# Kernel optimization log

Hardware: AMD Instinct MI355X
Metric: run time of the kernel (lower is better)

The kernel has to match this reference:

```python
import jax, jax.numpy as jnp
import numpy as np

N_NODES = 40000
N_EDGES = 640000
N_FEAT = 128
HIDDEN = 128
N_GRAPHS = 64


def _sage_conv(x, src, dst, Wl, b, Wr):
    # PyG SAGEConv (aggr='mean', root_weight=True, normalize=False):
    # out_i = W_l @ mean_{j in N(i)} x_j + b + W_r @ x_i
    msg = x[src]                                             # [E, F]
    s = jax.ops.segment_sum(msg, dst, num_segments=N_NODES)  # [N, F]
    deg = jax.ops.segment_sum(jnp.ones((src.shape[0],), x.dtype), dst,
                              num_segments=N_NODES)
    agg = s / jnp.maximum(deg, 1.0)[:, None]
    return agg @ Wl + b + x @ Wr


def setup_inputs() -> dict:
    key = jax.random.key(0)
    ks = jax.random.split(key, 12)
    sc = 1.0 / np.sqrt(N_FEAT)
    x = jax.random.normal(ks[0], (N_NODES, N_FEAT), dtype=jnp.float32)
    edge_index = jax.random.randint(ks[1], (2, N_EDGES), 0, N_NODES, dtype=jnp.int32)
    batch = jnp.sort(jax.random.randint(ks[2], (N_NODES,), 0, N_GRAPHS, dtype=jnp.int32))
    mk = lambda k, shp: (jax.random.normal(k, shp, dtype=jnp.float32) * sc)
    return {
        'x': x, 'edge_index': edge_index, 'batch': batch,
        'W1l': mk(ks[3], (N_FEAT, HIDDEN)), 'b1': jnp.zeros((HIDDEN,), jnp.float32),
        'W1r': mk(ks[4], (N_FEAT, HIDDEN)),
        'W2l': mk(ks[5], (HIDDEN, HIDDEN)), 'b2': jnp.zeros((HIDDEN,), jnp.float32),
        'W2r': mk(ks[6], (HIDDEN, HIDDEN)),
        'W3l': mk(ks[7], (HIDDEN, HIDDEN)), 'b3': jnp.zeros((HIDDEN,), jnp.float32),
        'W3r': mk(ks[8], (HIDDEN, HIDDEN)),
        'Wlin': mk(ks[9], (3 * HIDDEN, HIDDEN)), 'blin': jnp.zeros((HIDDEN,), jnp.float32),
    }


def reference(x, edge_index, batch, W1l, b1, W1r, W2l, b2, W2r, W3l, b3, W3r, Wlin, blin):
    src, dst = edge_index[0], edge_index[1]
    h1 = jax.nn.relu(_sage_conv(x, src, dst, W1l, b1, W1r))
    h2 = jax.nn.relu(_sage_conv(h1, src, dst, W2l, b2, W2r))
    h3 = jax.nn.relu(_sage_conv(h2, src, dst, W3l, b3, W3r))
    h = jnp.concatenate([h1, h2, h3], axis=1)                # [N, 3*H]
    pooled = jax.ops.segment_sum(h, batch, num_segments=N_GRAPHS)  # global_add_pool
    out = jax.nn.relu(pooled @ Wlin + blin)                  # [G, H]
    return out
```

## Files before the change

kernel.cpp:

```cpp
#include <hip/hip_runtime.h>
#include <hip/hip_bf16.h>

#define N_NODES 40000
#define N_EDGES 640000
#define NFEAT 128
#define NGRAPHS 64
#define ECAP 1024

typedef __attribute__((ext_vector_type(8))) short short8;
typedef __attribute__((ext_vector_type(4))) float float4v;
typedef __attribute__((ext_vector_type(2))) float float2v;

static __device__ __forceinline__ float bf2f(unsigned short u) {
    unsigned int x = ((unsigned int)u) << 16;
    return __builtin_bit_cast(float, x);
}
static __device__ __forceinline__ unsigned short f2bf(float f) {
    unsigned int x = __builtin_bit_cast(unsigned int, f);
    unsigned int r = x + 0x7fffu + ((x >> 16) & 1u);
    return (unsigned short)(r >> 16);
}

__global__ void k_prep(const int* __restrict__ dst, int* __restrict__ deg,
                       const int* __restrict__ batch, int* __restrict__ goff,
                       const float* __restrict__ x, unsigned short* __restrict__ h0,
                       const float* __restrict__ Wl0, const float* __restrict__ Wr0,
                       const float* __restrict__ Wl1, const float* __restrict__ Wr1,
                       const float* __restrict__ Wl2, const float* __restrict__ Wr2,
                       unsigned short* __restrict__ Wt, float* __restrict__ pooled) {
    int b = blockIdx.x;
    if (b < 2500) {
        int e = b * 256 + threadIdx.x;
        if (e < N_EDGES) atomicAdd(&deg[dst[e]], 1);
    } else if (b < 2657) {
        int i = (b - 2500) * 256 + threadIdx.x;
        if (i >= N_NODES) return;
        int b1 = batch[i];
        int b0 = (i == 0) ? -1 : batch[i - 1];
        for (int g = b0 + 1; g <= b1; ++g) goff[g] = i;
        if (i == N_NODES - 1)
            for (int g = b1 + 1; g <= NGRAPHS; ++g) goff[g] = N_NODES;
    } else if (b < 5157) {
        int i = (b - 2657) * 256 + threadIdx.x;
        const int n = N_NODES * NFEAT / 8;
        if (i < n) {
            const float4* xf = (const float4*)x;
            float4 p0 = xf[2 * i], p1 = xf[2 * i + 1];
            uint4 v;
            v.x = (unsigned int)f2bf(p0.x) | ((unsigned int)f2bf(p0.y) << 16);
            v.y = (unsigned int)f2bf(p0.z) | ((unsigned int)f2bf(p0.w) << 16);
            v.z = (unsigned int)f2bf(p1.x) | ((unsigned int)f2bf(p1.y) << 16);
            v.w = (unsigned int)f2bf(p1.z) | ((unsigned int)f2bf(p1.w) << 16);
            ((uint4*)h0)[i] = v;
        }
    } else if (b < 5541) {
        int id = (b - 5157) * 256 + threadIdx.x;
        if (id >= 3 * 128 * 256) return;
        int l   = id >> 15;
        int rem = id & 32767;
        int nn  = rem >> 8;
        int k   = rem & 255;
        const float* Wl = (l == 0) ? Wl0 : (l == 1) ? Wl1 : Wl2;
        const float* Wr = (l == 0) ? Wr0 : (l == 1) ? Wr1 : Wr2;
        float v = (k < 128) ? Wl[k * 128 + nn] : Wr[(k - 128) * 128 + nn];
        Wt[id] = f2bf(v);
    } else {
        int j = (b - 5541) * 256 + threadIdx.x;
        if (j < NGRAPHS * 384) pooled[j] = 0.f;
    }
}

__global__ __launch_bounds__(1024) void k_scan(const int* __restrict__ deg,
                                               int* __restrict__ offsets,
                                               int* __restrict__ cursor) {
    __shared__ int ws[16];
    __shared__ int s_boff;
    int tid = threadIdx.x;
    int b = blockIdx.x;
    int lane = tid & 63, wave = tid >> 6;

    int lim = b << 10;
    int s = 0;
    for (int i = tid; i < lim; i += 1024) s += deg[i];
    for (int d = 1; d < 64; d <<= 1) s += __shfl_xor(s, d, 64);
    if (lane == 0) ws[wave] = s;
    __syncthreads();
    if (tid == 0) {
        int t = 0;
        for (int w = 0; w < 16; ++w) t += ws[w];
        s_boff = t;
    }
    __syncthreads();
    int boff = s_boff;

    int i = (b << 10) + tid;
    int v = (i < N_NODES) ? deg[i] : 0;
    int incl = v;
    for (int d = 1; d < 64; d <<= 1) {
        int t = __shfl_up(incl, d, 64);
        if (lane >= d) incl += t;
    }
    __syncthreads();
    if (lane == 63) ws[wave] = incl;
    __syncthreads();
    if (wave == 0 && lane < 16) {
        int w = ws[lane];
        for (int d = 1; d < 16; d <<= 1) {
            int t = __shfl_up(w, d, 64);
            if (lane >= d) w += t;
        }
        ws[lane] = w;
    }
    __syncthreads();
    int waveOff = (wave == 0) ? 0 : ws[wave - 1];
    if (i < N_NODES) {
        int o = boff + waveOff + incl - v;
        offsets[i] = o;
        cursor[i]  = o;
    }
    if (b == 39 && tid == 0) offsets[N_NODES] = N_EDGES;
}

__global__ void k_fill(const int* __restrict__ src, const int* __restrict__ dst,
                       int* __restrict__ cursor, unsigned short* __restrict__ esrc) {
    int e = blockIdx.x * 256 + threadIdx.x;
    if (e < N_EDGES) {
        int d = dst[e];
        int p = atomicAdd(&cursor[d], 1);
        esrc[p] = (unsigned short)src[e];
    }
}

__global__ __launch_bounds__(256, 8) void k_sage(
        const unsigned short* __restrict__ hin,
        const int* __restrict__ offsets,
        const unsigned short* __restrict__ esrc,
        const int* __restrict__ batch,
        const unsigned short* __restrict__ Wt,
        const float* __restrict__ bias,
        unsigned short* __restrict__ hout,
        float* __restrict__ poolseg) {
    __shared__ __align__(16) unsigned short As[32][264];
    __shared__ __align__(16) unsigned short eidx[ECAP];
    int tid = threadIdx.x;
    int row0 = blockIdx.x * 32;

    int estart = offsets[row0];
    int ecnt   = offsets[row0 + 32] - estart;
    int staged = ecnt < ECAP ? ecnt : ECAP;

    for (int p = 0; p < 2; ++p) {
        int ci = tid + p * 256;
        int r = ci >> 4, c8 = ci & 15;
        uint4 v = *(const uint4*)(hin + (size_t)(row0 + r) * 128 + c8 * 8);
        *(uint4*)(&As[r][128 + c8 * 8]) = v;
    }
    for (int t = tid; t < staged; t += 256) eidx[t] = esrc[estart + t];
    __syncthreads();

    {
        int grp = tid >> 4;
        int sub = tid & 15;
        for (int nn = 0; nn < 2; ++nn) {
            int r = nn * 16 + grp;
            int node = row0 + r;
            int beg = offsets[node], end = offsets[node + 1];
            float2v a0 = {0.f, 0.f}, a1 = a0, a2 = a0, a3 = a0;
            auto acc8 = [&](uint4 u) {
                float2v t0, t1, t2, t3;
                t0.x = __builtin_bit_cast(float, u.x << 16);
                t0.y = __builtin_bit_cast(float, u.x & 0xffff0000u);
                t1.x = __builtin_bit_cast(float, u.y << 16);
                t1.y = __builtin_bit_cast(float, u.y & 0xffff0000u);
                t2.x = __builtin_bit_cast(float, u.z << 16);
                t2.y = __builtin_bit_cast(float, u.z & 0xffff0000u);
                t3.x = __builtin_bit_cast(float, u.w << 16);
                t3.y = __builtin_bit_cast(float, u.w & 0xffff0000u);
                a0 += t0; a1 += t1; a2 += t2; a3 += t3;
            };
            if (end - estart <= staged) {
                int lj = beg - estart, lend = end - estart;
                for (; lj + 8 <= lend; lj += 8) {
                    int s0 = eidx[lj],     s1 = eidx[lj + 1];
                    int s2 = eidx[lj + 2], s3 = eidx[lj + 3];
                    int s4 = eidx[lj + 4], s5 = eidx[lj + 5];
                    int s6 = eidx[lj + 6], s7 = eidx[lj + 7];
                    uint4 u0 = *(const uint4*)(hin + (size_t)s0 * 128 + sub * 8);
                    uint4 u1 = *(const uint4*)(hin + (size_t)s1 * 128 + sub * 8);
                    uint4 u2 = *(const uint4*)(hin + (size_t)s2 * 128 + sub * 8);
                    uint4 u3 = *(const uint4*)(hin + (size_t)s3 * 128 + sub * 8);
                    uint4 u4 = *(const uint4*)(hin + (size_t)s4 * 128 + sub * 8);
                    uint4 u5 = *(const uint4*)(hin + (size_t)s5 * 128 + sub * 8);
                    uint4 u6 = *(const uint4*)(hin + (size_t)s6 * 128 + sub * 8);
                    uint4 u7 = *(const uint4*)(hin + (size_t)s7 * 128 + sub * 8);
                    acc8(u0); acc8(u1); acc8(u2); acc8(u3);
                    acc8(u4); acc8(u5); acc8(u6); acc8(u7);
                }
                for (; lj < lend; ++lj) {
                    int s = eidx[lj];
                    uint4 u = *(const uint4*)(hin + (size_t)s * 128 + sub * 8);
                    acc8(u);
                }
            } else {
                for (int j = beg; j < end; ++j) {
                    int s = esrc[j];
                    uint4 u = *(const uint4*)(hin + (size_t)s * 128 + sub * 8);
                    acc8(u);
                }
            }
            int deg = end - beg;
            float inv = 1.f / (float)(deg > 1 ? deg : 1);
            uint4 v;
            v.x = (unsigned int)f2bf(a0.x * inv) | ((unsigned int)f2bf(a0.y * inv) << 16);
            v.y = (unsigned int)f2bf(a1.x * inv) | ((unsigned int)f2bf(a1.y * inv) << 16);
            v.z = (unsigned int)f2bf(a2.x * inv) | ((unsigned int)f2bf(a2.y * inv) << 16);
            v.w = (unsigned int)f2bf(a3.x * inv) | ((unsigned int)f2bf(a3.y * inv) << 16);
            *(uint4*)(&As[r][sub * 8]) = v;
        }
    }
    __syncthreads();

    int wave = tid >> 6, lane = tid & 63;
    int quad = lane >> 4, l16 = lane & 15;
    float4v acc[2][2];
    for (int rt = 0; rt < 2; ++rt)
        for (int ct = 0; ct < 2; ++ct) acc[rt][ct] = {0.f, 0.f, 0.f, 0.f};

    int ncol0 = wave * 32;
    for (int kc = 0; kc < 8; ++kc) {
        int k0 = kc * 32 + quad * 8;
        short8 a[2], b[2];
        for (int rt = 0; rt < 2; ++rt)
            a[rt] = *(const short8*)(&As[rt * 16 + l16][k0]);
        for (int ct = 0; ct < 2; ++ct)
            b[ct] = *(const short8*)(Wt + (size_t)(ncol0 + ct * 16 + l16) * 256 + k0);
        for (int rt = 0; rt < 2; ++rt)
            for (int ct = 0; ct < 2; ++ct)
                acc[rt][ct] = __builtin_amdgcn_mfma_f32_16x16x32_bf16(
                    a[rt], b[ct], acc[rt][ct], 0, 0, 0);
    }

    __syncthreads();
    float* Ps = (float*)&As[0][0];
    int* sbatch = (int*)&eidx[0];
    if (tid < 32) sbatch[tid] = batch[row0 + tid];

    for (int ct = 0; ct < 2; ++ct) {
        int col = ncol0 + ct * 16 + l16;
        float bv = bias[col];
        for (int rt = 0; rt < 2; ++rt) {
            int r0 = rt * 16 + quad * 4;
            for (int i = 0; i < 4; ++i) {
                float v = acc[rt][ct][i] + bv;
                v = v > 0.f ? v : 0.f;
                if (hout) hout[(size_t)(row0 + r0 + i) * 128 + col] = f2bf(v);
                Ps[(r0 + i) * 132 + col] = v;
            }
        }
    }
    __syncthreads();

    {
        int half = tid >> 7;
        int c = tid & 127;
        int rbase = half * 16;
        float accp = 0.f;
        int cur = sbatch[rbase];
        for (int r = rbase; r < rbase + 16; ++r) {
            int g = sbatch[r];
            if (g != cur) {
                atomicAdd(&poolseg[cur * 384 + c], accp);
                accp = 0.f;
                cur = g;
            }
            accp += Ps[r * 132 + c];
        }
        atomicAdd(&poolseg[cur * 384 + c], accp);
    }
}

__global__ void k_final(const float* __restrict__ pooled,
                        const float* __restrict__ Wlin,
                        const float* __restrict__ blin,
                        float* __restrict__ out) {
    __shared__ float part[128];
    int g = blockIdx.x;
    int t = threadIdx.x;
    int col = t & 127, half = t >> 7;
    int k0 = half * 192;
    float acc = 0.f;
    for (int k = k0; k < k0 + 192; ++k)
        acc = fmaf(pooled[g * 384 + k], Wlin[k * 128 + col], acc);
    if (half) part[col] = acc;
    __syncthreads();
    if (!half) {
        float v = acc + part[col] + blin[col];
        out[g * 128 + col] = v > 0.f ? v : 0.f;
    }
}

extern "C" void kernel_launch(void* const* d_in, const int* in_sizes, int n_in,
                              void* d_out, int out_size, void* d_ws, size_t ws_size,
                              hipStream_t stream) {
    const float* x    = (const float*)d_in[0];
    const int*   ei   = (const int*)d_in[1];
    const int*   src  = ei;
    const int*   dst  = ei + N_EDGES;
    const int*   batch = (const int*)d_in[2];
    const float* W1l = (const float*)d_in[3];
    const float* b1  = (const float*)d_in[4];
    const float* W1r = (const float*)d_in[5];
    const float* W2l = (const float*)d_in[6];
    const float* b2  = (const float*)d_in[7];
    const float* W2r = (const float*)d_in[8];
    const float* W3l = (const float*)d_in[9];
    const float* b3  = (const float*)d_in[10];
    const float* W3r = (const float*)d_in[11];
    const float* Wlin = (const float*)d_in[12];
    const float* blin = (const float*)d_in[13];
    float* out = (float*)d_out;

    char* ws = (char*)d_ws;
    size_t off = 0;
    auto alloc = [&](size_t bytes) -> char* {
        char* p = ws + off;
        off = (off + bytes + 255) & ~(size_t)255;
        return p;
    };
    int* offsets = (int*)alloc((N_NODES + 1) * sizeof(int));
    int* cursor  = (int*)alloc(N_NODES * sizeof(int));
    int* deg     = (int*)alloc(N_NODES * sizeof(int));
    int* goff    = (int*)alloc((NGRAPHS + 1) * sizeof(int));
    unsigned short* esrc = (unsigned short*)alloc(N_EDGES * sizeof(unsigned short));
    unsigned short* h0   = (unsigned short*)alloc((size_t)N_NODES * 128 * 2);
    unsigned short* h1   = (unsigned short*)alloc((size_t)N_NODES * 128 * 2);
    unsigned short* h2   = (unsigned short*)alloc((size_t)N_NODES * 128 * 2);
    unsigned short* Wt   = (unsigned short*)alloc(3 * 256 * 128 * 2);
    float* pooled = (float*)alloc(NGRAPHS * 384 * sizeof(float));

    hipMemsetAsync(deg, 0, N_NODES * sizeof(int), stream);

    k_prep<<<5637, 256, 0, stream>>>(dst, deg, batch, goff, x, h0,
                                     W1l, W1r, W2l, W2r, W3l, W3r, Wt, pooled);
    k_scan<<<40, 1024, 0, stream>>>(deg, offsets, cursor);
    k_fill<<<(N_EDGES + 255) / 256, 256, 0, stream>>>(src, dst, cursor, esrc);

    k_sage<<<1250, 256, 0, stream>>>(h0, offsets, esrc, batch, Wt,
                                     b1, h1, pooled);
    k_sage<<<1250, 256, 0, stream>>>(h1, offsets, esrc, batch, Wt + 32768,
                                     b2, h2, pooled + 128);
    k_sage<<<1250, 256, 0, stream>>>(h2, offsets, esrc, batch, Wt + 2 * 32768,
                                     b3, (unsigned short*)nullptr, pooled + 256);

    k_final<<<NGRAPHS, 256, 0, stream>>>(pooled, Wlin, blin, out);
}
```

Baseline: 255.9 us.

## Store node features in column-panel-major layout and gather per 32-column panel

Node features are now stored as four column panels of 32 bf16 values per node instead of contiguous 128-wide rows. The prep conversion, the self-feature staging, the neighbour gather and the hidden-output writes all use the new layout consistently. The gather now walks the edge list once per panel and loads 4 bytes per lane per edge rather than 16. The aim is better cache locality within each panel, at the cost of four times as many load instructions and index reads, plus 64-byte rather than 256-byte row segments per access.

```diff
diff --git a/kernel.cpp b/kernel.cpp
--- a/kernel.cpp
+++ b/kernel.cpp
@@ -6,6 +6,7 @@
 #define NFEAT 128
 #define NGRAPHS 64
 #define ECAP 1024
+
 
 typedef __attribute__((ext_vector_type(8))) short short8;
 typedef __attribute__((ext_vector_type(4))) float float4v;
@@ -51,7 +52,9 @@
             v.y = (unsigned int)f2bf(p0.z) | ((unsigned int)f2bf(p0.w) << 16);
             v.z = (unsigned int)f2bf(p1.x) | ((unsigned int)f2bf(p1.y) << 16);
             v.w = (unsigned int)f2bf(p1.z) | ((unsigned int)f2bf(p1.w) << 16);
-            ((uint4*)h0)[i] = v;
+            int node = i >> 4, c8 = i & 15;
+            int p = c8 >> 2;
+            ((uint4*)h0)[p * 160000 + node * 4 + (c8 & 3)] = v;
         }
     } else if (b < 5541) {
         int id = (b - 5157) * 256 + threadIdx.x;
@@ -149,10 +152,10 @@
     int ecnt   = offsets[row0 + 32] - estart;
     int staged = ecnt < ECAP ? ecnt : ECAP;
 
-    for (int p = 0; p < 2; ++p) {
-        int ci = tid + p * 256;
+    for (int pp = 0; pp < 2; ++pp) {
+        int ci = tid + pp * 256;
         int r = ci >> 4, c8 = ci & 15;
-        uint4 v = *(const uint4*)(hin + (size_t)(row0 + r) * 128 + c8 * 8);
+        uint4 v = ((const uint4*)hin)[(c8 >> 2) * 160000 + (size_t)(row0 + r) * 4 + (c8 & 3)];
         *(uint4*)(&As[r][128 + c8 * 8]) = v;
     }
     for (int t = tid; t < staged; t += 256) eidx[t] = esrc[estart + t];
@@ -161,61 +164,51 @@
     {
         int grp = tid >> 4;
         int sub = tid & 15;
+        const unsigned* hw = (const unsigned*)hin;
         for (int nn = 0; nn < 2; ++nn) {
             int r = nn * 16 + grp;
             int node = row0 + r;
             int beg = offsets[node], end = offsets[node + 1];
-            float2v a0 = {0.f, 0.f}, a1 = a0, a2 = a0, a3 = a0;
-            auto acc8 = [&](uint4 u) {
-                float2v t0, t1, t2, t3;
-                t0.x = __builtin_bit_cast(float, u.x << 16);
-                t0.y = __builtin_bit_cast(float, u.x & 0xffff0000u);
-                t1.x = __builtin_bit_cast(float, u.y << 16);
-                t1.y = __builtin_bit_cast(float, u.y & 0xffff0000u);
-                t2.x = __builtin_bit_cast(float, u.z << 16);
-                t2.y = __builtin_bit_cast(float, u.z & 0xffff0000u);
-                t3.x = __builtin_bit_cast(float, u.w << 16);
-                t3.y = __builtin_bit_cast(float, u.w & 0xffff0000u);
-                a0 += t0; a1 += t1; a2 += t2; a3 += t3;
-            };
-            if (end - estart <= staged) {
-                int lj = beg - estart, lend = end - estart;
-                for (; lj + 8 <= lend; lj += 8) {
-                    int s0 = eidx[lj],     s1 = eidx[lj + 1];
-                    int s2 = eidx[lj + 2], s3 = eidx[lj + 3];
-                    int s4 = eidx[lj + 4], s5 = eidx[lj + 5];
-                    int s6 = eidx[lj + 6], s7 = eidx[lj + 7];
-                    uint4 u0 = *(const uint4*)(hin + (size_t)s0 * 128 + sub * 8);
-                    uint4 u1 = *(const uint4*)(hin + (size_t)s1 * 128 + sub * 8);
-                    uint4 u2 = *(const uint4*)(hin + (size_t)s2 * 128 + sub * 8);
-                    uint4 u3 = *(const uint4*)(hin + (size_t)s3 * 128 + sub * 8);
-                    uint4 u4 = *(const uint4*)(hin + (size_t)s4 * 128 + sub * 8);
-                    uint4 u5 = *(const uint4*)(hin + (size_t)s5 * 128 + sub * 8);
-                    uint4 u6 = *(const uint4*)(hin + (size_t)s6 * 128 + sub * 8);
-                    uint4 u7 = *(const uint4*)(hin + (size_t)s7 * 128 + sub * 8);
-                    acc8(u0); acc8(u1); acc8(u2); acc8(u3);
-                    acc8(u4); acc8(u5); acc8(u6); acc8(u7);
-                }
-                for (; lj < lend; ++lj) {
-                    int s = eidx[lj];
-                    uint4 u = *(const uint4*)(hin + (size_t)s * 128 + sub * 8);
-                    acc8(u);
-                }
-            } else {
-                for (int j = beg; j < end; ++j) {
-                    int s = esrc[j];
-                    uint4 u = *(const uint4*)(hin + (size_t)s * 128 + sub * 8);
-                    acc8(u);
-                }
-            }
             int deg = end - beg;
             float inv = 1.f / (float)(deg > 1 ? deg : 1);
-            uint4 v;
-            v.x = (unsigned int)f2bf(a0.x * inv) | ((unsigned int)f2bf(a0.y * inv) << 16);
-            v.y = (unsigned int)f2bf(a1.x * inv) | ((unsigned int)f2bf(a1.y * inv) << 16);
-            v.z = (unsigned int)f2bf(a2.x * inv) | ((unsigned int)f2bf(a2.y * inv) << 16);
-            v.w = (unsigned int)f2bf(a3.x * inv) | ((unsigned int)f2bf(a3.y * inv) << 16);
-            *(uint4*)(&As[r][sub * 8]) = v;
+            bool fast = (end - estart <= staged);
+            for (int p = 0; p < 4; ++p) {
+                int pbase = p * 640000 + sub;
+                float2v a = {0.f, 0.f};
+                auto accw = [&](unsigned u) {
+                    float2v t;
+                    t.x = __builtin_bit_cast(float, u << 16);
+                    t.y = __builtin_bit_cast(float, u & 0xffff0000u);
+                    a += t;
+                };
+                if (fast) {
+                    int lj = beg - estart, lend = end - estart;
+                    for (; lj + 8 <= lend; lj += 8) {
+                        int s0 = eidx[lj],     s1 = eidx[lj + 1];
+                        int s2 = eidx[lj + 2], s3 = eidx[lj + 3];
+                        int s4 = eidx[lj + 4], s5 = eidx[lj + 5];
+                        int s6 = eidx[lj + 6], s7 = eidx[lj + 7];
+                        unsigned u0 = hw[pbase + s0 * 16];
+                        unsigned u1 = hw[pbase + s1 * 16];
+                        unsigned u2 = hw[pbase + s2 * 16];
+                        unsigned u3 = hw[pbase + s3 * 16];
+                        unsigned u4 = hw[pbase + s4 * 16];
+                        unsigned u5 = hw[pbase + s5 * 16];
+                        unsigned u6 = hw[pbase + s6 * 16];
+                        unsigned u7 = hw[pbase + s7 * 16];
+                        accw(u0); accw(u1); accw(u2); accw(u3);
+                        accw(u4); accw(u5); accw(u6); accw(u7);
+                    }
+                    for (; lj < lend; ++lj)
+                        accw(hw[pbase + (int)eidx[lj] * 16]);
+                } else {
+                    for (int j = beg; j < end; ++j)
+                        accw(hw[pbase + (int)esrc[j] * 16]);
+                }
+                unsigned o = (unsigned)f2bf(a.x * inv) |
+                             ((unsigned)f2bf(a.y * inv) << 16);
+                *(unsigned*)(&As[r][p * 32 + sub * 2]) = o;
+            }
         }
     }
     __syncthreads();
@@ -248,12 +241,14 @@
     for (int ct = 0; ct < 2; ++ct) {
         int col = ncol0 + ct * 16 + l16;
         float bv = bias[col];
+        int pnl = col >> 5, cin = col & 31;
         for (int rt = 0; rt < 2; ++rt) {
             int r0 = rt * 16 + quad * 4;
             for (int i = 0; i < 4; ++i) {
                 float v = acc[rt][ct][i] + bv;
                 v = v > 0.f ? v : 0.f;
-                if (hout) hout[(size_t)(row0 + r0 + i) * 128 + col] = f2bf(v);
+                if (hout)
+                    hout[((size_t)pnl * N_NODES + (row0 + r0 + i)) * 32 + cin] = f2bf(v);
                 Ps[(r0 + i) * 132 + col] = v;
             }
         }
```

After: 299.5 us. +17.0%, slower.
